# Optimization experiments

Hardware: AMD Instinct MI355X
Metric: run time of the kernel (lower is better)

Reference implementation:

```python
import jax, jax.numpy as jnp
import numpy as np
from jax import lax

SR = 4      # sr_ratio
HEADS = 8   # num_heads


def _upsample_bilinear_ac(x, out_h, out_w):
    # torch nn.Upsample(scale_factor=SR, mode='bilinear', align_corners=True)
    B, C, h, w = x.shape
    ys = jnp.linspace(0.0, h - 1.0, out_h)
    xs = jnp.linspace(0.0, w - 1.0, out_w)
    y0 = jnp.floor(ys).astype(jnp.int32)
    y1 = jnp.minimum(y0 + 1, h - 1)
    wy = (ys - y0).astype(x.dtype)
    x0 = jnp.floor(xs).astype(jnp.int32)
    x1 = jnp.minimum(x0 + 1, w - 1)
    wx = (xs - x0).astype(x.dtype)
    r = x[:, :, y0, :] * (1.0 - wy)[None, None, :, None] + x[:, :, y1, :] * wy[None, None, :, None]
    return r[:, :, :, x0] * (1.0 - wx) + r[:, :, :, x1] * wx


def _forward(x, sr_w, sr_b, ln_g, ln_b, q_w, k1_w, v1_w, k2_w, v2_w, proj_w, proj_b):
    B, C, H, W = x.shape
    ID = C // 4                      # internal_dim
    hd = ID // HEADS                 # head_dim
    scale = float(hd) ** -0.5
    # spatial-reduction conv for Q path: [B, ID, H/4, W/4]
    qf = lax.conv_general_dilated(x, sr_w, (SR, SR), 'VALID',
                                  dimension_numbers=('NCHW', 'OIHW', 'NCHW'))
    qf = qf + sr_b[None, :, None, None]
    Hs, Ws = qf.shape[2], qf.shape[3]
    N = Hs * Ws
    qf = qf.reshape(B, ID, N).transpose(0, 2, 1)          # [B, N, ID]
    # LayerNorm
    mu = qf.mean(-1, keepdims=True)
    var = qf.var(-1, keepdims=True)
    qn = (qf - mu) / jnp.sqrt(var + 1e-5) * ln_g + ln_b
    q = qn @ q_w                                          # [B, N, ID]
    # max / avg pooled K,V inputs: [B, N, C]
    xm = lax.reduce_window(x, -jnp.inf, lax.max, (1, 1, SR, SR), (1, 1, SR, SR), 'VALID')
    xm = xm.reshape(B, C, N).transpose(0, 2, 1)
    xa = lax.reduce_window(x, 0.0, lax.add, (1, 1, SR, SR), (1, 1, SR, SR), 'VALID') / float(SR * SR)
    xa = xa.reshape(B, C, N).transpose(0, 2, 1)

    def heads(t):
        return t.reshape(B, N, HEADS, hd).transpose(0, 2, 1, 3)  # [B, H, N, hd]

    qh = heads(q)
    k1, v1 = heads(xm @ k1_w), heads(xm @ v1_w)
    k2, v2 = heads(xa @ k2_w), heads(xa @ v2_w)

    def attend(k, v):
        a = jax.nn.softmax(jnp.einsum('bhnd,bhmd->bhnm', qh, k) * scale, axis=-1)
        return jnp.einsum('bhnm,bhmd->bhnd', a, v)

    z = attend(k1, v1) + attend(k2, v2)                   # [B, H, N, hd]
    z = z.transpose(0, 2, 1, 3).reshape(B, N, ID)
    z = z @ proj_w + proj_b                               # [B, N, C]
    z = z.transpose(0, 2, 1).reshape(B, C, Hs, Ws)
    return _upsample_bilinear_ac(z, H, W)


def setup_inputs() -> dict:
    key = jax.random.key(0)
    ks = jax.random.split(key, 9)
    B, C, H, W = 16, 256, 112, 112
    ID = C // 4

    def n(k, shape, s=0.02):
        return jax.random.normal(k, shape, jnp.float32) * s

    return {
        'x': jax.random.normal(ks[0], (B, C, H, W), jnp.float32),
        'sr_w': n(ks[1], (ID, C, SR, SR)),
        'sr_b': jnp.zeros((ID,), jnp.float32),
        'ln_g': jnp.ones((ID,), jnp.float32),
        'ln_b': jnp.zeros((ID,), jnp.float32),
        'q_w': n(ks[2], (ID, ID)),
        'k1_w': n(ks[3], (C, ID)),
        'v1_w': n(ks[4], (C, ID)),
        'k2_w': n(ks[5], (C, ID)),
        'v2_w': n(ks[6], (C, ID)),
        'proj_w': n(ks[7], (ID, C)),
        'proj_b': jnp.zeros((C,), jnp.float32),
    }


def reference(x, sr_w, sr_b, ln_g, ln_b, q_w, k1_w, v1_w, k2_w, v2_w, proj_w, proj_b):
    return _forward(x, sr_w, sr_b, ln_g, ln_b, q_w, k1_w, v1_w, k2_w, v2_w, proj_w, proj_b)
```

## Files before the change

kernel.cpp:

```cpp
#include <hip/hip_runtime.h>
#include <math.h>

typedef __attribute__((ext_vector_type(8))) short short8;
typedef __attribute__((ext_vector_type(4))) short bh4;
typedef __attribute__((ext_vector_type(4))) float f32x4;
typedef __attribute__((ext_vector_type(2))) unsigned uint2v;
typedef __attribute__((ext_vector_type(4))) unsigned uint4v;

#define MFMA16(A,B,C) __builtin_amdgcn_mfma_f32_16x16x32_bf16(A,B,C,0,0,0)

#if __has_builtin(__builtin_amdgcn_mfma_f32_16x16x16bf16_1k)
#define MFMA16x16(A,B,C) __builtin_amdgcn_mfma_f32_16x16x16bf16_1k(A,B,C,0,0,0)
#else
__device__ __forceinline__ f32x4 mfma16x16_asm(bh4 a, bh4 b, f32x4 c){
    asm volatile("v_mfma_f32_16x16x16_bf16 %0, %1, %2, %0" : "+v"(c) : "v"(a), "v"(b));
    return c;
}
#define MFMA16x16(A,B,C) mfma16x16_asm(A,B,C)
#endif

__device__ __forceinline__ unsigned short f2b(float f){
    unsigned u = __builtin_bit_cast(unsigned, f);
    return (unsigned short)((u + 0x7fffu + ((u>>16)&1u)) >> 16);
}
__device__ __forceinline__ unsigned pk2(float a, float b){
    return (unsigned)f2b(a) | ((unsigned)f2b(b) << 16);
}
__device__ __forceinline__ unsigned pk2rn(float a, float b){
    unsigned ua = __builtin_bit_cast(unsigned, a) + 0x8000u;
    unsigned ub = __builtin_bit_cast(unsigned, b) + 0x8000u;
    return (ua >> 16) | (ub & 0xffff0000u);
}


__global__ __launch_bounds__(256) void ktw(const float* __restrict__ srw,
    const float* __restrict__ qw, const float* __restrict__ k1w,
    const float* __restrict__ v1w, const float* __restrict__ k2w,
    const float* __restrict__ v2w, char* __restrict__ srwb,
    char* __restrict__ Wtm, char* __restrict__ Wta, char* __restrict__ QWt)
{
    int blk = blockIdx.x, t = threadIdx.x;
    if (blk < 128){
        int base = blk*2048 + t*8;
        float4 a = *(const float4*)(srw + base);
        float4 b = *(const float4*)(srw + base + 4);
        uint4 u = { pk2(a.x,a.y), pk2(a.z,a.w), pk2(b.x,b.y), pk2(b.z,b.w) };
        *(uint4*)(srwb + (size_t)base*2) = u;
    } else if (blk < 136){
        __shared__ float T[256*33];
        int idx = blk - 128, fi = idx >> 1, half = idx & 1;
        const float* src = (fi==0) ? k1w : (fi==1) ? v1w : (fi==2) ? k2w : v2w;
        char* dst = ((fi < 2) ? Wtm : Wta) + (size_t)((fi & 1)*64 + half*32) * 512;
        for (int li = t; li < 8192; li += 256){
            int c = li >> 5, o = li & 31;
            T[c*33 + o] = src[c*64 + half*32 + o];
        }
        __syncthreads();
        for (int lo = t; lo < 1024; lo += 256){
            int o = lo >> 5, c8 = lo & 31;
            float v[8];
            #pragma unroll
            for (int k = 0; k < 8; ++k) v[k] = T[(c8*8 + k)*33 + o];
            uint4 u = { pk2(v[0],v[1]), pk2(v[2],v[3]), pk2(v[4],v[5]), pk2(v[6],v[7]) };
            *(uint4*)(dst + o*512 + c8*16) = u;
        }
    } else {
        __shared__ float T[64*65];
        for (int li = t; li < 4096; li += 256)
            T[(li >> 6)*65 + (li & 63)] = qw[li];
        __syncthreads();
        for (int lo = t; lo < 512; lo += 256){
            int o = lo >> 3, i8 = lo & 7;
            float v[8];
            #pragma unroll
            for (int k = 0; k < 8; ++k) v[k] = T[(i8*8 + k)*65 + o];
            uint4 u = { pk2(v[0],v[1]), pk2(v[2],v[3]), pk2(v[4],v[5]), pk2(v[6],v[7]) };
            *(uint4*)(QWt + o*128 + i8*16) = u;
        }
    }
}

__global__ __launch_bounds__(512, 3) void k1(const float* __restrict__ x,
    const char* __restrict__ srwb, char* __restrict__ R, float* __restrict__ pws)
{
    __shared__ float pm[28*66];
    __shared__ float pa[28*66];
    int blk = blockIdx.x;
    int b = blk / 112, r5 = blk % 112, hs = r5 >> 2, cg4 = r5 & 3;
    int t = threadIdx.x;
    int w = t >> 6, l = t & 63, lr = l & 15, lg = l >> 4;
    int ofr = w & 3, kh = w >> 2;
    int ks0 = kh*16;
    int cpar = lg >> 1, r0 = (lg & 1) * 2;
    f32x4 acc0 = {0.f,0.f,0.f,0.f}, acc1 = {0.f,0.f,0.f,0.f};
    const float* xc = x + (size_t)(b*256 + cg4*64)*12544 + (size_t)(hs*4 + r0)*112;
    const char* Brow = srwb + (size_t)(ofr*16 + lr)*8192 + cg4*2048 + lg*16;
    int p0 = lr, p1 = min(16 + lr, 27);
    bool poolw = (ofr == 0);

    f32x4 A0,A1,A2,A3; uint4v Ba;
    f32x4 C0,C1,C2,C3; uint4v Bc;
    f32x4 D0,D1,D2,D3; uint4v Bd;
    f32x4 E0,E1,E2,E3; uint4v Be;

#define ISSUE(Xa,Xb,Xc,Xd,Bv,KS) do{ \
    const float* _s = xc + (size_t)((KS)*2 + cpar)*12544; \
    const char*  _bp = Brow + (KS)*64; \
    asm volatile("global_load_dwordx4 %0, %1, off" : "=&v"(Xa) : "v"(_s + p0*4)); \
    asm volatile("global_load_dwordx4 %0, %1, off" : "=&v"(Xb) : "v"(_s + 112 + p0*4)); \
    asm volatile("global_load_dwordx4 %0, %1, off" : "=&v"(Xc) : "v"(_s + p1*4)); \
    asm volatile("global_load_dwordx4 %0, %1, off" : "=&v"(Xd) : "v"(_s + 112 + p1*4)); \
    asm volatile("global_load_dwordx4 %0, %1, off" : "=&v"(Bv) : "v"(_bp)); }while(0)

#define WAITN(N) do{ asm volatile("s_waitcnt vmcnt(" #N ")" ::: "memory"); \
                     __builtin_amdgcn_sched_barrier(0); }while(0)

#define COMP(Xa,Xb,Xc,Xd,Bv,KS) do{ \
    if (poolw){ \
        float mx0 = fmaxf(fmaxf(fmaxf(Xa[0],Xa[1]),fmaxf(Xa[2],Xa[3])), \
                          fmaxf(fmaxf(Xb[0],Xb[1]),fmaxf(Xb[2],Xb[3]))); \
        float sm0 = (Xa[0]+Xa[1])+(Xa[2]+Xa[3])+(Xb[0]+Xb[1])+(Xb[2]+Xb[3]); \
        float mx1 = fmaxf(fmaxf(fmaxf(Xc[0],Xc[1]),fmaxf(Xc[2],Xc[3])), \
                          fmaxf(fmaxf(Xd[0],Xd[1]),fmaxf(Xd[2],Xd[3]))); \
        float sm1 = (Xc[0]+Xc[1])+(Xc[2]+Xc[3])+(Xd[0]+Xd[1])+(Xd[2]+Xd[3]); \
        mx0 = fmaxf(mx0, __shfl_xor(mx0, 16, 64)); \
        sm0 = sm0 + __shfl_xor(sm0, 16, 64); \
        mx1 = fmaxf(mx1, __shfl_xor(mx1, 16, 64)); \
        sm1 = sm1 + __shfl_xor(sm1, 16, 64); \
        if ((lg & 1) == 0){ \
            int c = (KS)*2 + cpar; \
            pm[p0*66 + c] = mx0; pa[p0*66 + c] = sm0 * (1.f/16.f); \
            if (lr < 12){ pm[p1*66 + c] = mx1; pa[p1*66 + c] = sm1 * (1.f/16.f); } \
        } \
    } \
    short8 af0 = __builtin_bit_cast(short8, \
        (uint4v){ pk2(Xa[0],Xa[1]), pk2(Xa[2],Xa[3]), pk2(Xb[0],Xb[1]), pk2(Xb[2],Xb[3]) }); \
    short8 af1 = __builtin_bit_cast(short8, \
        (uint4v){ pk2(Xc[0],Xc[1]), pk2(Xc[2],Xc[3]), pk2(Xd[0],Xd[1]), pk2(Xd[2],Xd[3]) }); \
    short8 bf = __builtin_bit_cast(short8, Bv); \
    acc0 = MFMA16(af0, bf, acc0); \
    acc1 = MFMA16(af1, bf, acc1); }while(0)

    ISSUE(A0,A1,A2,A3,Ba, ks0+0);
    ISSUE(C0,C1,C2,C3,Bc, ks0+1);
    ISSUE(D0,D1,D2,D3,Bd, ks0+2);
    ISSUE(E0,E1,E2,E3,Be, ks0+3);
    #pragma unroll 1
    for (int it = 0; it < 3; ++it){
        int s4 = ks0 + it*4;
        WAITN(15); COMP(A0,A1,A2,A3,Ba, s4+0); ISSUE(A0,A1,A2,A3,Ba, s4+4);
        WAITN(15); COMP(C0,C1,C2,C3,Bc, s4+1); ISSUE(C0,C1,C2,C3,Bc, s4+5);
        WAITN(15); COMP(D0,D1,D2,D3,Bd, s4+2); ISSUE(D0,D1,D2,D3,Bd, s4+6);
        WAITN(15); COMP(E0,E1,E2,E3,Be, s4+3); ISSUE(E0,E1,E2,E3,Be, s4+7);
    }
    WAITN(15); COMP(A0,A1,A2,A3,Ba, ks0+12);
    WAITN(10); COMP(C0,C1,C2,C3,Bc, ks0+13);
    WAITN(5);  COMP(D0,D1,D2,D3,Bd, ks0+14);
    WAITN(0);  COMP(E0,E1,E2,E3,Be, ks0+15);

#undef ISSUE
#undef WAITN
#undef COMP

    size_t rowB = (size_t)b*784 + hs*28;
    float* pp = pws + (size_t)(((b*28 + hs)*4 + cg4)*2 + kh)*1792;
    #pragma unroll
    for (int rg = 0; rg < 4; ++rg){
        int m0 = lg*4 + rg, m1 = 16 + lg*4 + rg;
        pp[m0*64 + ofr*16 + lr] = acc0[rg];
        if (m1 < 28) pp[m1*64 + ofr*16 + lr] = acc1[rg];
    }
    __syncthreads();
    if (t < 224){
        int m = t >> 3, sub = t & 7;
        float vm[8], va8[8];
        #pragma unroll
        for (int k = 0; k < 8; ++k){
            vm[k]  = pm[m*66 + sub*8 + k];
            va8[k] = pa[m*66 + sub*8 + k];
        }
        uint4 um = { pk2(vm[0],vm[1]), pk2(vm[2],vm[3]), pk2(vm[4],vm[5]), pk2(vm[6],vm[7]) };
        uint4 ua = { pk2(va8[0],va8[1]), pk2(va8[2],va8[3]), pk2(va8[4],va8[5]), pk2(va8[6],va8[7]) };
        *(uint4*)(R + (rowB + m)*1024 + cg4*128 + sub*16)       = um;
        *(uint4*)(R + (rowB + m)*1024 + 512 + cg4*128 + sub*16) = ua;
    }
}

__global__ __launch_bounds__(512) void k2(const float* __restrict__ pws_,
    const float* __restrict__ srb, const float* __restrict__ lng,
    const float* __restrict__ lnb, const char* __restrict__ Wtm,
    const char* __restrict__ Wta, const char* __restrict__ QWt,
    char* __restrict__ R)
{
    __shared__ __align__(16) char PM[16384];
    __shared__ __align__(16) char PA[16384];
    __shared__ float Db[32*64];
    __shared__ __align__(16) char QN[4096];
    int blk = blockIdx.x, b = blk/28, hs = blk%28;
    int t = threadIdx.x, w = t>>6, l = t&63, lr = l&15, lg = l>>4;
    size_t rowB = (size_t)b*784 + hs*28;
    const char* Rb = R + rowB*1024;
    for (int li = t; li < 896; li += 512){
        int m = li >> 5, c16 = li & 31;
        uint4 vm = *(const uint4*)(Rb + (size_t)m*1024 + c16*16);
        uint4 va = *(const uint4*)(Rb + (size_t)m*1024 + 512 + c16*16);
        int dst = m*512 + ((c16*16) ^ ((m&7)<<4));
        *(uint4*)(PM + dst) = vm;
        *(uint4*)(PA + dst) = va;
    }
    const float* p0 = pws_ + (size_t)(b*28 + hs)*8*1792;
    for (int e = t; e < 1792; e += 512)
        Db[e] = (((p0[e] + p0[1792+e]) + (p0[3584+e] + p0[5376+e]))
              + ((p0[7168+e] + p0[8960+e]) + (p0[10752+e] + p0[12544+e]))) + srb[e & 63];
    __syncthreads();
    float g = lng[l], be = lnb[l];
    #pragma unroll
    for (int i = 0; i < 4; ++i){
        int m = w + i*8;
        float v = Db[m*64 + l];
        float s = v, ss = v*v;
        #pragma unroll
        for (int off = 1; off < 64; off <<= 1){
            s  += __shfl_xor(s,  off, 64);
            ss += __shfl_xor(ss, off, 64);
        }
        float mu = s * (1.f/64.f);
        float var = ss * (1.f/64.f) - mu*mu;
        float qn = (v - mu) * rsqrtf(var + 1e-5f) * g + be;
        *(unsigned short*)(QN + m*128 + ((l*2) ^ ((m&7)<<4))) = f2b(qn);
    }
    __syncthreads();
    int fam = w >> 2, ofp = w & 3;
    const char* PMA = fam ? PA : PM;
    const char* Wt  = fam ? Wta : Wtm;
    f32x4 a00={0.f,0.f,0.f,0.f}, a01=a00, a10=a00, a11=a00;
    int swzr = (lr & 7) << 4;
    #pragma unroll
    for (int ks = 0; ks < 8; ++ks){
        int kb = ks*64 + lg*16;
        short8 x0 = *(const short8*)(PMA + lr*512 + (kb ^ swzr));
        short8 x1 = *(const short8*)(PMA + (16+lr)*512 + (kb ^ swzr));
        short8 b0 = *(const short8*)(Wt + (size_t)(ofp*32 + lr)*512 + kb);
        short8 b1 = *(const short8*)(Wt + (size_t)(ofp*32 + 16 + lr)*512 + kb);
        a00 = MFMA16(x0, b0, a00); a01 = MFMA16(x0, b1, a01);
        a10 = MFMA16(x1, b0, a10); a11 = MFMA16(x1, b1, a11);
    }
    f32x4 q0={0.f,0.f,0.f,0.f}, q1=q0;
    if (w < 4){
        #pragma unroll
        for (int ks = 0; ks < 2; ++ks){
            int kb = ks*64 + lg*16;
            short8 xa_ = *(const short8*)(QN + lr*128 + (kb ^ swzr));
            short8 xb_ = *(const short8*)(QN + (16+lr)*128 + (kb ^ swzr));
            short8 bq  = *(const short8*)(QWt + (size_t)(w*16 + lr)*128 + kb);
            q0 = MFMA16(xa_, bq, q0);
            q1 = MFMA16(xb_, bq, q1);
        }
    }
    #pragma unroll
    for (int j = 0; j < 2; ++j){
        int o128 = ofp*32 + j*16 + lr;
        int o = o128 & 63, hh = o >> 3, dd = o & 7, mat = fam*2 + (o128 >> 6);
        int byteoff = 128 + hh*64 + mat*16 + dd*2;
        f32x4 am  = j ? a01 : a00;
        f32x4 am1 = j ? a11 : a10;
        #pragma unroll
        for (int rg = 0; rg < 4; ++rg){
            int m0 = lg*4 + rg, m1 = 16 + lg*4 + rg;
            *(unsigned short*)(R + (rowB + m0)*1024 + byteoff) = f2b(am[rg]);
            if (m1 < 28)
                *(unsigned short*)(R + (rowB + m1)*1024 + byteoff) = f2b(am1[rg]);
        }
    }
    if (w < 4){
        int o = w*16 + lr;
        #pragma unroll
        for (int rg = 0; rg < 4; ++rg){
            int m0 = lg*4 + rg, m1 = 16 + lg*4 + rg;
            *(unsigned short*)(R + (rowB + m0)*1024 + o*2) = f2b(q0[rg]);
            if (m1 < 28)
                *(unsigned short*)(R + (rowB + m1)*1024 + o*2) = f2b(q1[rg]);
        }
    }
}

__global__ __launch_bounds__(256) void kattn(const char* __restrict__ R, float* __restrict__ z)
{
    __shared__ __align__(16) char QT [6144];
    __shared__ __align__(16) char K1b[5376];
    __shared__ __align__(16) char K2b[5376];
    __shared__ __align__(16) char VT1[3840];
    __shared__ __align__(16) char VT2[3840];
    int blk = blockIdx.x;
    int bh = blk / 7, nseg = blk % 7;
    int b = bh >> 3, h = bh & 7;
    int t = threadIdx.x, w = t >> 6, l = t & 63;
    int col = l & 15, g = l >> 4;

    for (int i = t; i < 384; i += 256) ((uint4*)QT)[i] = uint4{0,0,0,0};
    for (int i = t; i < 112; i += 256){
        *(uint4*)(K1b + i*48 + 16) = uint4{0,0,0,0};
        *(uint4*)(K2b + i*48 + 16) = uint4{0,0,0,0};
    }
    for (int i = t; i < 120; i += 256){
        *(uint4*)(VT1 + 1920 + i*16) = uint4{0,0,0,0};
        *(uint4*)(VT2 + 1920 + i*16) = uint4{0,0,0,0};
    }
    __syncthreads();
    if (t < 112){
        uint4 qv = *(const uint4*)(R + ((size_t)b*784 + nseg*112 + t)*1024 + h*16);
        *(uint2*)(QT + t*48)     = uint2{qv.x, qv.y};
        *(uint2*)(QT + t*48 + 8) = uint2{qv.z, qv.w};
    }
    __syncthreads();

    bh4 qf[2];
    #pragma unroll
    for (int nf = 0; nf < 2; ++nf)
        qf[nf] = *(const bh4*)(QT + (w*28 + nf*16 + col)*48 + g*8);

    f32x4 o1[2] = {{0,0,0,0},{0,0,0,0}}, o2[2] = {{0,0,0,0},{0,0,0,0}};
    float d1[2] = {0.f,0.f}, d2[2] = {0.f,0.f};
    const float C2 = 0.51004244f;

    for (int mt = 0; mt < 7; ++mt){
        __syncthreads();
        for (int li = t; li < 448; li += 256){
            int m = li >> 2, part = li & 3;
            uint4 v = *(const uint4*)(R + ((size_t)b*784 + mt*112 + m)*1024 + 128 + h*64 + part*16);
            if ((part & 1) == 0){
                char* Kb = (part == 0) ? K1b : K2b;
                *(uint2*)(Kb + m*48)     = uint2{v.x, v.y};
                *(uint2*)(Kb + m*48 + 8) = uint2{v.z, v.w};
            } else {
                char* Vb = (part == 1) ? VT1 : VT2;
                unsigned arr[4] = {v.x, v.y, v.z, v.w};
                #pragma unroll
                for (int d = 0; d < 4; ++d){
                    *(unsigned short*)(Vb + (d*2)*240   + m*2) = (unsigned short)(arr[d] & 0xffffu);
                    *(unsigned short*)(Vb + (d*2+1)*240 + m*2) = (unsigned short)(arr[d] >> 16);
                }
            }
        }
        __syncthreads();
        #pragma unroll
        for (int mc = 0; mc < 7; ++mc){
            bh4 ka = *(const bh4*)(K1b + (mc*16 + col)*48 + g*8);
            bh4 kb = *(const bh4*)(K2b + (mc*16 + col)*48 + g*8);
            bh4 va = *(const bh4*)(VT1 + col*240 + mc*32 + g*8);
            bh4 vb = *(const bh4*)(VT2 + col*240 + mc*32 + g*8);
            #pragma unroll
            for (int nf = 0; nf < 2; ++nf){
                f32x4 zr = {0.f,0.f,0.f,0.f};
                f32x4 s1 = MFMA16x16(ka, qf[nf], zr);
                float p0 = exp2f(s1[0]*C2), p1 = exp2f(s1[1]*C2);
                float p2 = exp2f(s1[2]*C2), p3 = exp2f(s1[3]*C2);
                d1[nf] += (p0+p1)+(p2+p3);
                bh4 pf1 = __builtin_bit_cast(bh4, (uint2v){pk2rn(p0,p1), pk2rn(p2,p3)});
                o1[nf] = MFMA16x16(va, pf1, o1[nf]);
                f32x4 s2 = MFMA16x16(kb, qf[nf], zr);
                float r0 = exp2f(s2[0]*C2), r1 = exp2f(s2[1]*C2);
                float r2 = exp2f(s2[2]*C2), r3 = exp2f(s2[3]*C2);
                d2[nf] += (r0+r1)+(r2+r3);
                bh4 pf2 = __builtin_bit_cast(bh4, (uint2v){pk2rn(r0,r1), pk2rn(r2,r3)});
                o2[nf] = MFMA16x16(vb, pf2, o2[nf]);
            }
        }
    }
    #pragma unroll
    for (int nf = 0; nf < 2; ++nf){
        d1[nf] += __shfl_xor(d1[nf], 16, 64); d1[nf] += __shfl_xor(d1[nf], 32, 64);
        d2[nf] += __shfl_xor(d2[nf], 16, 64); d2[nf] += __shfl_xor(d2[nf], 32, 64);
    }
    if (g < 2){
        #pragma unroll
        for (int nf = 0; nf < 2; ++nf){
            if (nf == 1 && col >= 12) continue;
            int n = nseg*112 + w*28 + nf*16 + col;
            float ra = 1.f / d1[nf], rb = 1.f / d2[nf];
            float4 ov;
            ov.x = o1[nf][0]*ra + o2[nf][0]*rb;
            ov.y = o1[nf][1]*ra + o2[nf][1]*rb;
            ov.z = o1[nf][2]*ra + o2[nf][2]*rb;
            ov.w = o1[nf][3]*ra + o2[nf][3]*rb;
            *(float4*)(z + ((size_t)b*784 + n)*64 + h*8 + g*4) = ov;
        }
    }
}

__global__ __launch_bounds__(256) void kpu(const float* __restrict__ z,
    const float* __restrict__ pw, const float* __restrict__ pb,
    float* __restrict__ out)
{
    __shared__ float plane[8*784];
    __shared__ float wsl[64*8];
    __shared__ int   ti0[112];
    __shared__ float twv[112];
    int blk = blockIdx.x;
    int b = blk >> 5, cg = blk & 31;
    int t = threadIdx.x;
    if (t < 128){
        #pragma unroll
        for (int q = 0; q < 4; ++q){
            int idx = t*4 + q; int o = idx >> 3, j = idx & 7;
            wsl[o*8 + j] = pw[o*256 + cg*8 + j];
        }
    }
    if (t < 112){
        float s = (float)t * (27.f/111.f);
        int i0 = (int)s; if (i0 > 27) i0 = 27;
        ti0[t] = i0; twv[t] = s - (float)i0;
    }
    __syncthreads();
    {
        int nh = t >> 1, jh = (t & 1) * 4;
        float bias0 = pb[cg*8 + jh], bias1 = pb[cg*8 + jh + 1];
        float bias2 = pb[cg*8 + jh + 2], bias3 = pb[cg*8 + jh + 3];
        for (int n = nh; n < 784; n += 128){
            const float* zr = z + ((size_t)b*784 + n)*64;
            float a0 = bias0, a1 = bias1, a2 = bias2, a3 = bias3;
            #pragma unroll
            for (int o4 = 0; o4 < 16; ++o4){
                float4 zv = *(const float4*)(zr + o4*4);
                const float* wr = wsl + (o4*4)*8 + jh;
                a0 = fmaf(zv.x, wr[0],  a0); a1 = fmaf(zv.x, wr[1],  a1);
                a2 = fmaf(zv.x, wr[2],  a2); a3 = fmaf(zv.x, wr[3],  a3);
                a0 = fmaf(zv.y, wr[8],  a0); a1 = fmaf(zv.y, wr[9],  a1);
                a2 = fmaf(zv.y, wr[10], a2); a3 = fmaf(zv.y, wr[11], a3);
                a0 = fmaf(zv.z, wr[16], a0); a1 = fmaf(zv.z, wr[17], a1);
                a2 = fmaf(zv.z, wr[18], a2); a3 = fmaf(zv.z, wr[19], a3);
                a0 = fmaf(zv.w, wr[24], a0); a1 = fmaf(zv.w, wr[25], a1);
                a2 = fmaf(zv.w, wr[26], a2); a3 = fmaf(zv.w, wr[27], a3);
            }
            plane[(jh+0)*784 + n] = a0;
            plane[(jh+1)*784 + n] = a1;
            plane[(jh+2)*784 + n] = a2;
            plane[(jh+3)*784 + n] = a3;
        }
    }
    __syncthreads();
    float* ob = out + ((size_t)b*256 + cg*8)*12544;
    for (int i4 = t; i4 < 3136; i4 += 256){
        int y = i4 / 28, xq = (i4 % 28) * 4;
        int y0 = ti0[y], y1 = min(y0+1, 27);
        float wy = twv[y];
        int x0q[4], x1q[4]; float wxq[4];
        #pragma unroll
        for (int qi = 0; qi < 4; ++qi){
            int xx = xq + qi;
            x0q[qi] = ti0[xx]; x1q[qi] = min(x0q[qi]+1, 27); wxq[qi] = twv[xx];
        }
        int base = y*112 + xq;
        #pragma unroll
        for (int j = 0; j < 8; ++j){
            const float* r0p = plane + j*784 + y0*28;
            const float* r1p = plane + j*784 + y1*28;
            float4 ov;
            #pragma unroll
            for (int qi = 0; qi < 4; ++qi){
                float a  = r0p[x0q[qi]] + (r1p[x0q[qi]] - r0p[x0q[qi]])*wy;
                float bb = r0p[x1q[qi]] + (r1p[x1q[qi]] - r0p[x1q[qi]])*wy;
                float v = a + (bb - a)*wxq[qi];
                if (qi == 0) ov.x = v; else if (qi == 1) ov.y = v;
                else if (qi == 2) ov.z = v; else ov.w = v;
            }
            *(float4*)(ob + (size_t)j*12544 + base) = ov;
        }
    }
}

extern "C" void kernel_launch(void* const* d_in, const int* in_sizes, int n_in,
                              void* d_out, int out_size, void* d_ws, size_t ws_size,
                              hipStream_t stream) {
    const float* x   = (const float*)d_in[0];
    const float* srw = (const float*)d_in[1];
    const float* srb = (const float*)d_in[2];
    const float* lng = (const float*)d_in[3];
    const float* lnb = (const float*)d_in[4];
    const float* qw  = (const float*)d_in[5];
    const float* k1w = (const float*)d_in[6];
    const float* v1w = (const float*)d_in[7];
    const float* k2w = (const float*)d_in[8];
    const float* v2w = (const float*)d_in[9];
    const float* pw  = (const float*)d_in[10];
    const float* pb  = (const float*)d_in[11];

    char*  Rws  = (char*)d_ws;
    float* pws  = (float*)(Rws + 12845056);
    char*  srwb = Rws + 38535168;
    char*  Wtm  = Rws + 39059456;
    char*  Wta  = Rws + 39124992;
    char*  QWt  = Rws + 39190528;
    float* z    = (float*)(Rws + 12845056);
    float* out  = (float*)d_out;

    ktw  <<<137,  256, 0, stream>>>(srw, qw, k1w, v1w, k2w, v2w, srwb, Wtm, Wta, QWt);
    k1   <<<1792, 512, 0, stream>>>(x, srwb, Rws, pws);
    k2   <<<448,  512, 0, stream>>>(pws, srb, lng, lnb, Wtm, Wta, QWt, Rws);
    kattn<<<896,  256, 0, stream>>>(Rws, z);
    kpu  <<<512,  256, 0, stream>>>(z, pw, pb, out);
}
```

Baseline: 267.2 us.

## Restructure conv kernel so each wave owns channels and reduces partials in LDS

The spatial-reduction conv kernel now uses 256-thread blocks over 32 channels. Each wave covers 8 input channels and all four output-fragment groups, with the weight fragments preloaded into registers. Previously four waves loaded the same x tiles for different output fragments; now each x tile is read once per block and feeds four MFMA pairs. The four wave partials are summed in shared memory before writing the same number of partial slices as before. The cost is a larger shared-memory buffer, more accumulator registers, and extra barriers.

```diff
diff --git a/kernel.cpp b/kernel.cpp
--- a/kernel.cpp
+++ b/kernel.cpp
@@ -80,43 +80,50 @@
     }
 }
 
-__global__ __launch_bounds__(512, 3) void k1(const float* __restrict__ x,
+__global__ __launch_bounds__(256, 3) void k1(const float* __restrict__ x,
     const char* __restrict__ srwb, char* __restrict__ R, float* __restrict__ pws)
 {
-    __shared__ float pm[28*66];
-    __shared__ float pa[28*66];
+    __shared__ float pm[28*34];
+    __shared__ float pa[28*34];
+    __shared__ float red[4*2048];
     int blk = blockIdx.x;
-    int b = blk / 112, r5 = blk % 112, hs = r5 >> 2, cg4 = r5 & 3;
+    int b = blk / 224, r5 = blk % 224, hs = r5 >> 3, cg8 = r5 & 7;
     int t = threadIdx.x;
     int w = t >> 6, l = t & 63, lr = l & 15, lg = l >> 4;
-    int ofr = w & 3, kh = w >> 2;
-    int ks0 = kh*16;
     int cpar = lg >> 1, r0 = (lg & 1) * 2;
-    f32x4 acc0 = {0.f,0.f,0.f,0.f}, acc1 = {0.f,0.f,0.f,0.f};
-    const float* xc = x + (size_t)(b*256 + cg4*64)*12544 + (size_t)(hs*4 + r0)*112;
-    const char* Brow = srwb + (size_t)(ofr*16 + lr)*8192 + cg4*2048 + lg*16;
     int p0 = lr, p1 = min(16 + lr, 27);
-    bool poolw = (ofr == 0);
-
-    f32x4 A0,A1,A2,A3; uint4v Ba;
-    f32x4 C0,C1,C2,C3; uint4v Bc;
-    f32x4 D0,D1,D2,D3; uint4v Bd;
-    f32x4 E0,E1,E2,E3; uint4v Be;
-
-#define ISSUE(Xa,Xb,Xc,Xd,Bv,KS) do{ \
-    const float* _s = xc + (size_t)((KS)*2 + cpar)*12544; \
-    const char*  _bp = Brow + (KS)*64; \
+    int cb = cg8*32 + w*8;
+    const float* xc = x + (size_t)(b*256 + cb)*12544 + (size_t)(hs*4 + r0)*112;
+    const char* Bb = srwb + (size_t)lr*8192 + (size_t)cb*32 + lg*16;
+
+    uint4v Bf[4][4];
+    #pragma unroll
+    for (int s = 0; s < 4; ++s){
+        #pragma unroll
+        for (int f = 0; f < 4; ++f){
+            const char* bp = Bb + (size_t)f*131072 + s*64;
+            asm volatile("global_load_dwordx4 %0, %1, off" : "=&v"(Bf[s][f]) : "v"(bp));
+        }
+    }
+
+    f32x4 acc[4][2];
+    #pragma unroll
+    for (int f = 0; f < 4; ++f){ acc[f][0] = (f32x4){0.f,0.f,0.f,0.f}; acc[f][1] = (f32x4){0.f,0.f,0.f,0.f}; }
+
+    f32x4 A0,A1,A2,A3, C0,C1,C2,C3;
+
+#define ISSUEX(Xa,Xb,Xc,Xd,S) do{ \
+    const float* _s = xc + (size_t)((S)*2 + cpar)*12544; \
     asm volatile("global_load_dwordx4 %0, %1, off" : "=&v"(Xa) : "v"(_s + p0*4)); \
     asm volatile("global_load_dwordx4 %0, %1, off" : "=&v"(Xb) : "v"(_s + 112 + p0*4)); \
     asm volatile("global_load_dwordx4 %0, %1, off" : "=&v"(Xc) : "v"(_s + p1*4)); \
-    asm volatile("global_load_dwordx4 %0, %1, off" : "=&v"(Xd) : "v"(_s + 112 + p1*4)); \
-    asm volatile("global_load_dwordx4 %0, %1, off" : "=&v"(Bv) : "v"(_bp)); }while(0)
+    asm volatile("global_load_dwordx4 %0, %1, off" : "=&v"(Xd) : "v"(_s + 112 + p1*4)); }while(0)
 
 #define WAITN(N) do{ asm volatile("s_waitcnt vmcnt(" #N ")" ::: "memory"); \
                      __builtin_amdgcn_sched_barrier(0); }while(0)
 
-#define COMP(Xa,Xb,Xc,Xd,Bv,KS) do{ \
-    if (poolw){ \
+#define COMP(Xa,Xb,Xc,Xd,S) do{ \
+    { \
         float mx0 = fmaxf(fmaxf(fmaxf(Xa[0],Xa[1]),fmaxf(Xa[2],Xa[3])), \
                           fmaxf(fmaxf(Xb[0],Xb[1]),fmaxf(Xb[2],Xb[3]))); \
         float sm0 = (Xa[0]+Xa[1])+(Xa[2]+Xa[3])+(Xb[0]+Xb[1])+(Xb[2]+Xb[3]); \
@@ -128,61 +135,63 @@
         mx1 = fmaxf(mx1, __shfl_xor(mx1, 16, 64)); \
         sm1 = sm1 + __shfl_xor(sm1, 16, 64); \
         if ((lg & 1) == 0){ \
-            int c = (KS)*2 + cpar; \
-            pm[p0*66 + c] = mx0; pa[p0*66 + c] = sm0 * (1.f/16.f); \
-            if (lr < 12){ pm[p1*66 + c] = mx1; pa[p1*66 + c] = sm1 * (1.f/16.f); } \
+            int c = w*8 + (S)*2 + cpar; \
+            pm[p0*34 + c] = mx0; pa[p0*34 + c] = sm0 * (1.f/16.f); \
+            if (lr < 12){ pm[p1*34 + c] = mx1; pa[p1*34 + c] = sm1 * (1.f/16.f); } \
         } \
     } \
     short8 af0 = __builtin_bit_cast(short8, \
         (uint4v){ pk2(Xa[0],Xa[1]), pk2(Xa[2],Xa[3]), pk2(Xb[0],Xb[1]), pk2(Xb[2],Xb[3]) }); \
     short8 af1 = __builtin_bit_cast(short8, \
         (uint4v){ pk2(Xc[0],Xc[1]), pk2(Xc[2],Xc[3]), pk2(Xd[0],Xd[1]), pk2(Xd[2],Xd[3]) }); \
-    short8 bf = __builtin_bit_cast(short8, Bv); \
-    acc0 = MFMA16(af0, bf, acc0); \
-    acc1 = MFMA16(af1, bf, acc1); }while(0)
-
-    ISSUE(A0,A1,A2,A3,Ba, ks0+0);
-    ISSUE(C0,C1,C2,C3,Bc, ks0+1);
-    ISSUE(D0,D1,D2,D3,Bd, ks0+2);
-    ISSUE(E0,E1,E2,E3,Be, ks0+3);
-    #pragma unroll 1
-    for (int it = 0; it < 3; ++it){
-        int s4 = ks0 + it*4;
-        WAITN(15); COMP(A0,A1,A2,A3,Ba, s4+0); ISSUE(A0,A1,A2,A3,Ba, s4+4);
-        WAITN(15); COMP(C0,C1,C2,C3,Bc, s4+1); ISSUE(C0,C1,C2,C3,Bc, s4+5);
-        WAITN(15); COMP(D0,D1,D2,D3,Bd, s4+2); ISSUE(D0,D1,D2,D3,Bd, s4+6);
-        WAITN(15); COMP(E0,E1,E2,E3,Be, s4+3); ISSUE(E0,E1,E2,E3,Be, s4+7);
-    }
-    WAITN(15); COMP(A0,A1,A2,A3,Ba, ks0+12);
-    WAITN(10); COMP(C0,C1,C2,C3,Bc, ks0+13);
-    WAITN(5);  COMP(D0,D1,D2,D3,Bd, ks0+14);
-    WAITN(0);  COMP(E0,E1,E2,E3,Be, ks0+15);
-
-#undef ISSUE
+    _Pragma("unroll") for (int f = 0; f < 4; ++f){ \
+        short8 bf = __builtin_bit_cast(short8, Bf[S][f]); \
+        acc[f][0] = MFMA16(af0, bf, acc[f][0]); \
+        acc[f][1] = MFMA16(af1, bf, acc[f][1]); } }while(0)
+
+    ISSUEX(A0,A1,A2,A3, 0);
+    ISSUEX(C0,C1,C2,C3, 1);
+    WAITN(4); COMP(A0,A1,A2,A3, 0); ISSUEX(A0,A1,A2,A3, 2);
+    WAITN(4); COMP(C0,C1,C2,C3, 1); ISSUEX(C0,C1,C2,C3, 3);
+    WAITN(4); COMP(A0,A1,A2,A3, 2);
+    WAITN(0); COMP(C0,C1,C2,C3, 3);
+
+#undef ISSUEX
 #undef WAITN
 #undef COMP
 
+    __syncthreads();
+    {
+        float* wb = red + w*2048;
+        #pragma unroll
+        for (int f = 0; f < 4; ++f){
+            #pragma unroll
+            for (int rg = 0; rg < 4; ++rg){
+                int m0 = lg*4 + rg, m1 = 16 + lg*4 + rg;
+                wb[m0*64 + f*16 + lr] = acc[f][0][rg];
+                if (m1 < 28) wb[m1*64 + f*16 + lr] = acc[f][1][rg];
+            }
+        }
+    }
+    __syncthreads();
     size_t rowB = (size_t)b*784 + hs*28;
-    float* pp = pws + (size_t)(((b*28 + hs)*4 + cg4)*2 + kh)*1792;
-    #pragma unroll
-    for (int rg = 0; rg < 4; ++rg){
-        int m0 = lg*4 + rg, m1 = 16 + lg*4 + rg;
-        pp[m0*64 + ofr*16 + lr] = acc0[rg];
-        if (m1 < 28) pp[m1*64 + ofr*16 + lr] = acc1[rg];
-    }
-    __syncthreads();
-    if (t < 224){
-        int m = t >> 3, sub = t & 7;
+    {
+        float* pp = pws + (size_t)((b*28 + hs)*8 + cg8)*1792;
+        for (int e = t; e < 1792; e += 256)
+            pp[e] = (red[e] + red[2048 + e]) + (red[4096 + e] + red[6144 + e]);
+    }
+    if (t < 112){
+        int m = t >> 2, sub = t & 3;
         float vm[8], va8[8];
         #pragma unroll
         for (int k = 0; k < 8; ++k){
-            vm[k]  = pm[m*66 + sub*8 + k];
-            va8[k] = pa[m*66 + sub*8 + k];
+            vm[k]  = pm[m*34 + sub*8 + k];
+            va8[k] = pa[m*34 + sub*8 + k];
         }
         uint4 um = { pk2(vm[0],vm[1]), pk2(vm[2],vm[3]), pk2(vm[4],vm[5]), pk2(vm[6],vm[7]) };
         uint4 ua = { pk2(va8[0],va8[1]), pk2(va8[2],va8[3]), pk2(va8[4],va8[5]), pk2(va8[6],va8[7]) };
-        *(uint4*)(R + (rowB + m)*1024 + cg4*128 + sub*16)       = um;
-        *(uint4*)(R + (rowB + m)*1024 + 512 + cg4*128 + sub*16) = ua;
+        *(uint4*)(R + (rowB + m)*1024 + cg8*64 + sub*16)       = um;
+        *(uint4*)(R + (rowB + m)*1024 + 512 + cg8*64 + sub*16) = ua;
     }
 }
 
@@ -495,7 +504,7 @@
     float* out  = (float*)d_out;
 
     ktw  <<<137,  256, 0, stream>>>(srw, qw, k1w, v1w, k2w, v2w, srwb, Wtm, Wta, QWt);
-    k1   <<<1792, 512, 0, stream>>>(x, srwb, Rws, pws);
+    k1   <<<3584, 256, 0, stream>>>(x, srwb, Rws, pws);
     k2   <<<448,  512, 0, stream>>>(pws, srb, lng, lnb, Wtm, Wta, QWt, Rws);
     kattn<<<896,  256, 0, stream>>>(Rws, z);
     kpu  <<<512,  256, 0, stream>>>(z, pw, pb, out);
```

Measured after the change: 239.5 us. 10.4% less time.
